# Kernel optimization log

Hardware: AMD Instinct MI355X
Metric: run time of the kernel (lower is better)

## Reference

```python
import jax, jax.numpy as jnp
import numpy as np

HEAD_SIZE = 64

def setup_inputs() -> dict:
    key = jax.random.key(0)
    kx, kk, kq, kv = jax.random.split(key, 4)
    B, T, C, H = 8, 2048, 1024, HEAD_SIZE
    scale = 1.0 / np.sqrt(C)
    x = jax.random.normal(kx, (B, T, C), dtype=jnp.float32)
    # nn.Linear(n_emb, head_size, bias=False) weights, shape (head_size, n_emb)
    Wk = jax.random.normal(kk, (H, C), dtype=jnp.float32) * scale
    Wq = jax.random.normal(kq, (H, C), dtype=jnp.float32) * scale
    Wv = jax.random.normal(kv, (H, C), dtype=jnp.float32) * scale
    return {"x": x, "Wk": Wk, "Wq": Wq, "Wv": Wv}

def reference(x, Wk, Wq, Wv):
    # x: (B,T,C); W*: (H,C). Single causal self-attention head.
    H = Wk.shape[0]
    k = jnp.einsum('btc,hc->bth', x, Wk)
    q = jnp.einsum('btc,hc->bth', x, Wq)
    v = jnp.einsum('btc,hc->bth', x, Wv)
    scores = jnp.einsum('bth,bsh->bts', q, k) / jnp.sqrt(jnp.float32(H))
    T = x.shape[1]
    causal = jnp.tril(jnp.ones((T, T), dtype=bool))  # (T,T)
    scores = jnp.where(causal, scores, -jnp.inf)
    attn = jax.nn.softmax(scores, axis=-1)
    out = jnp.einsum('bts,bsh->bth', attn, v)  # (B,T,H)
    return out
```

## Files before the change

### kernel.cpp

```cpp
#include <hip/hip_runtime.h>
#include <hip/hip_bf16.h>

typedef __bf16 bf16_t;
typedef __bf16 bf16x8 __attribute__((ext_vector_type(8)));
typedef float  f32x4  __attribute__((ext_vector_type(4)));

#define B_ 8
#define T_ 2048
#define C_ 1024
#define H_ 64

#define MFMA16(a, b, c) __builtin_amdgcn_mfma_f32_16x16x32_bf16((a), (b), (c), 0, 0, 0)
#define GLL16(g, l) __builtin_amdgcn_global_load_lds( \
    (const __attribute__((address_space(1))) unsigned int*)(g), \
    (__attribute__((address_space(3))) unsigned int*)(l), 16, 0, 0)
#define SBAR() asm volatile("s_barrier" ::: "memory")

__global__ __launch_bounds__(256) void wconv_kernel(
    const float* __restrict__ Wk, const float* __restrict__ Wq,
    const float* __restrict__ Wv,
    bf16_t* __restrict__ Wh, bf16_t* __restrict__ Wl,
    f32x4* __restrict__ zero_dst)
{
    int i = blockIdx.x * 256 + threadIdx.x;
    zero_dst[i] = (f32x4){0.f, 0.f, 0.f, 0.f};
    if (blockIdx.x < 768) {
        int r = i >> 10;
        int c = i & 1023;
        float v;
        if (r < 64)       v = Wq[r * 1024 + c];
        else if (r < 128) v = Wk[(r - 64) * 1024 + c];
        else              v = Wv[(r - 128) * 1024 + c];
        bf16_t h = (bf16_t)v;
        Wh[i] = h;
        Wl[i] = (bf16_t)(v - (float)h);
    }
}

__global__ __launch_bounds__(512, 2) void proj_kernel(
    const float*  __restrict__ x,
    const bf16_t* __restrict__ Wh, const bf16_t* __restrict__ Wl,
    bf16_t* __restrict__ qh, bf16_t* __restrict__ ql,
    bf16_t* __restrict__ kh, bf16_t* __restrict__ kl,
    bf16_t* __restrict__ vh)
{
    __shared__ bf16_t Wlds[2][48][512];

    const int tid   = threadIdx.x;
    const int wid   = tid >> 6;
    const int lane  = tid & 63;
    const int quad  = lane >> 4;
    const int l16   = lane & 15;
    const int mhalf = wid >> 1;
    const int nhalf = wid & 1;
    const int g     = blockIdx.x * 64 + mhalf * 16 + l16;
    const float* xrow = x + (size_t)g * C_;

    auto stage = [&](int k0, int bufi) {
        #pragma unroll
        for (int i = 0; i < 6; ++i) {
            int grp  = wid * 6 + i;
            int ksub = (grp >= 24);
            int rem  = grp - ksub * 24;
            int mat  = (rem >= 12);
            int nt   = rem - mat * 12;
            const bf16_t* src = (mat ? Wl : Wh)
                + (nt * 16 + l16) * 1024 + k0 + ksub * 32 + quad * 8;
            GLL16(src, &Wlds[bufi][grp][0]);
        }
    };
    auto loadx = [&](int it, f32x4* d) {
        #pragma unroll
        for (int ks = 0; ks < 2; ++ks) {
            d[ks * 2]     = *(const f32x4*)(xrow + it * 64 + ks * 32 + quad * 8);
            d[ks * 2 + 1] = *(const f32x4*)(xrow + it * 64 + ks * 32 + quad * 8 + 4);
        }
    };

    stage(0, 0);
    f32x4 x0[4], x1[4];
    loadx(0, x0);
    loadx(1, x1);

    f32x4 acc[6];
    #pragma unroll
    for (int i = 0; i < 6; ++i) acc[i] = (f32x4){0.f, 0.f, 0.f, 0.f};

    int buf = 0;
    for (int it = 0; it < 16; ++it) {
        float xv[16];
        *(f32x4*)(xv)      = x0[0];
        *(f32x4*)(xv + 4)  = x0[1];
        *(f32x4*)(xv + 8)  = x0[2];
        *(f32x4*)(xv + 12) = x0[3];
        #pragma unroll
        for (int i = 0; i < 4; ++i) x0[i] = x1[i];

        if (it + 1 < 16) {
            stage((it + 1) * 64, buf ^ 1);
            if (it + 2 < 16) {
                loadx(it + 2, x1);
                asm volatile("s_waitcnt vmcnt(10)" ::: "memory");
            } else {
                asm volatile("s_waitcnt vmcnt(6)" ::: "memory");
            }
        } else {
            asm volatile("s_waitcnt vmcnt(0)" ::: "memory");
        }
        SBAR();

        #pragma unroll
        for (int ks = 0; ks < 2; ++ks) {
            bf16x8 ah, al;
            #pragma unroll
            for (int jj = 0; jj < 8; ++jj) {
                float  xf = xv[ks * 8 + jj];
                bf16_t h  = (bf16_t)xf;
                ah[jj] = h;
                al[jj] = (bf16_t)(xf - (float)h);
            }
            #pragma unroll
            for (int nt = 0; nt < 6; ++nt) {
                int gi = ks * 24 + nhalf * 6 + nt;
                bf16x8 bh = *(const bf16x8*)(&Wlds[buf][gi][lane * 8]);
                bf16x8 bl = *(const bf16x8*)(&Wlds[buf][gi + 12][lane * 8]);
                acc[nt] = MFMA16(ah, bh, acc[nt]);
                acc[nt] = MFMA16(ah, bl, acc[nt]);
                acc[nt] = MFMA16(al, bh, acc[nt]);
            }
        }

        SBAR();
        buf ^= 1;
    }

    const int rowbase = blockIdx.x * 64 + mhalf * 16 + quad * 4;
    for (int nt = 0; nt < 6; ++nt) {
        int n = (nhalf * 6 + nt) * 16 + l16;
        for (int rr = 0; rr < 4; ++rr) {
            int grow = rowbase + rr;
            int bb = grow >> 11, t = grow & 2047;
            float v  = acc[nt][rr];
            bf16_t h = (bf16_t)v;
            if (n < 64) {
                int off = (bb * T_ + t) * H_ + n;
                qh[off] = h; ql[off] = (bf16_t)(v - (float)h);
            } else if (n < 128) {
                int off = (bb * T_ + t) * H_ + (n - 64);
                kh[off] = h; kl[off] = (bf16_t)(v - (float)h);
            } else {
                vh[(bb * H_ + (n - 128)) * T_ + t] = h;
            }
        }
    }
}

__global__ __launch_bounds__(512, 4) void attn_kernel(
    const bf16_t* __restrict__ qh, const bf16_t* __restrict__ ql,
    const bf16_t* __restrict__ kh, const bf16_t* __restrict__ kl,
    const bf16_t* __restrict__ vh,
    float* __restrict__ Oacc, float* __restrict__ lacc)
{
    __shared__ bf16_t KV[2][3][4096];
    __shared__ bf16_t Plds[8][16 * 72];

    const int tid  = threadIdx.x;
    const int wid  = tid >> 6;
    const int lane = tid & 63;
    const int quad = lane >> 4;
    const int l16  = lane & 15;

    const int b  = blockIdx.x & 7;
    const int gp = (blockIdx.x >> 3) & 7;
    const int s  = blockIdx.x >> 6;
    const int gA = gp, gB = 15 - gp;
    const int nA = 2 * gA + 2;

    const int t_nt   = wid >> 1;
    const int t_kk   = wid & 1;
    const int t_l16  = tid & 15;
    const int t_quad = (tid >> 4) & 3;
    const int koff   = (t_nt * 16 + t_l16) * H_ + t_kk * 32 + t_quad * 8;
    const int voff   = (t_nt * 16 + t_l16) * T_ + t_kk * 32 + t_quad * 8;

    auto stage = [&](int j, int bufi) {
        const size_t kbase = (size_t)(b * T_ + 64 * j) * H_;
        GLL16(kh + kbase + koff, &KV[bufi][0][wid * 512]);
        GLL16(kl + kbase + koff, &KV[bufi][1][wid * 512]);
        GLL16(vh + (size_t)b * H_ * T_ + 64 * j + voff, &KV[bufi][2][wid * 512]);
    };

    f32x4  O[4];
    float  rowsum[4];
    bf16x8 aqh[2], aql[2];
    int    gcur = -1;

    auto flushO = [&]() {
        #pragma unroll
        for (int rr = 0; rr < 4; ++rr) {
            int trow = b * T_ + 128 * gcur + 16 * wid + quad * 4 + rr;
            #pragma unroll
            for (int ht = 0; ht < 4; ++ht)
                atomicAdd(Oacc + (size_t)trow * H_ + ht * 16 + l16, O[ht][rr]);
            float s_ = rowsum[rr];
            s_ += __shfl_xor(s_, 1, 64);
            s_ += __shfl_xor(s_, 2, 64);
            s_ += __shfl_xor(s_, 4, 64);
            s_ += __shfl_xor(s_, 8, 64);
            if (l16 == 0) atomicAdd(lacc + trow, s_);
        }
    };

    {
        int u0 = s;
        int j0 = (u0 < nA) ? u0 : (u0 - nA);
        stage(j0, 0);
    }

    int buf = 0;
    for (int u = s; u < 34; u += 8) {
        const int g = (u < nA) ? gA : gB;
        const int j = (u < nA) ? u : (u - nA);

        const int un = u + 8;
        if (un < 34) {
            int jn = (un < nA) ? un : (un - nA);
            stage(jn, buf ^ 1);
            asm volatile("s_waitcnt vmcnt(3)" ::: "memory");
        } else {
            asm volatile("s_waitcnt vmcnt(0)" ::: "memory");
        }
        SBAR();

        if (g != gcur) {
            if (gcur >= 0) flushO();
            gcur = g;
            const size_t qoff = (size_t)(b * T_ + 128 * g + 16 * wid + l16) * H_;
            #pragma unroll
            for (int kk = 0; kk < 2; ++kk) {
                aqh[kk] = *(const bf16x8*)(qh + qoff + kk * 32 + quad * 8);
                aql[kk] = *(const bf16x8*)(ql + qoff + kk * 32 + quad * 8);
            }
            #pragma unroll
            for (int i = 0; i < 4; ++i) { O[i] = (f32x4){0.f,0.f,0.f,0.f}; rowsum[i] = 0.f; }
        }

        const bf16_t* Kh = KV[buf][0];
        const bf16_t* Kl = KV[buf][1];
        f32x4 S[4];
        #pragma unroll
        for (int i = 0; i < 4; ++i) S[i] = (f32x4){0.f,0.f,0.f,0.f};
        #pragma unroll
        for (int nt = 0; nt < 4; ++nt) {
            #pragma unroll
            for (int kk = 0; kk < 2; ++kk) {
                bf16x8 bh = *(const bf16x8*)(Kh + (nt * 2 + kk) * 512 + lane * 8);
                bf16x8 bl = *(const bf16x8*)(Kl + (nt * 2 + kk) * 512 + lane * 8);
                S[nt] = MFMA16(aqh[kk], bh, S[nt]);
                S[nt] = MFMA16(aqh[kk], bl, S[nt]);
                S[nt] = MFMA16(aql[kk], bh, S[nt]);
            }
        }

        bf16_t* Pw = Plds[wid];
        const int rloc = 128 * g + 16 * wid + quad * 4;
        #pragma unroll
        for (int nt = 0; nt < 4; ++nt) {
            int colt = 64 * j + nt * 16 + l16;
            #pragma unroll
            for (int rr = 0; rr < 4; ++rr) {
                float pv = (colt <= rloc + rr)
                         ? __expf(fmaf(S[nt][rr], 0.125f, -20.0f)) : 0.f;
                rowsum[rr] += pv;
                Pw[(quad * 4 + rr) * 72 + nt * 16 + l16] = (bf16_t)pv;
            }
        }

        bf16x8 ap0 = *(const bf16x8*)(Pw + l16 * 72 + quad * 8);
        bf16x8 ap1 = *(const bf16x8*)(Pw + l16 * 72 + 32 + quad * 8);

        const bf16_t* Vt = KV[buf][2];
        #pragma unroll
        for (int ht = 0; ht < 4; ++ht) {
            bf16x8 bv0 = *(const bf16x8*)(Vt + (ht * 2 + 0) * 512 + lane * 8);
            bf16x8 bv1 = *(const bf16x8*)(Vt + (ht * 2 + 1) * 512 + lane * 8);
            O[ht] = MFMA16(ap0, bv0, O[ht]);
            O[ht] = MFMA16(ap1, bv1, O[ht]);
        }

        SBAR();
        buf ^= 1;
    }
    if (gcur >= 0) flushO();
}

__global__ __launch_bounds__(256) void div_kernel(
    const float* __restrict__ Oacc, const float* __restrict__ lacc,
    float* __restrict__ out)
{
    int i = blockIdx.x * 256 + threadIdx.x;
    f32x4 o   = ((const f32x4*)Oacc)[i];
    float inv = 1.0f / lacc[i >> 4];
    ((f32x4*)out)[i] = o * inv;
}

extern "C" void kernel_launch(void* const* d_in, const int* in_sizes, int n_in,
                              void* d_out, int out_size, void* d_ws, size_t ws_size,
                              hipStream_t stream)
{
    const float* x  = (const float*)d_in[0];
    const float* Wk = (const float*)d_in[1];
    const float* Wq = (const float*)d_in[2];
    const float* Wv = (const float*)d_in[3];
    float* out = (float*)d_out;

    char* ws = (char*)d_ws;
    const size_t WSZ = 192 * 1024 * sizeof(bf16_t);
    const size_t QSZ = (size_t)B_ * T_ * H_ * sizeof(bf16_t);
    bf16_t* Wh   = (bf16_t*)(ws);
    bf16_t* Wl   = (bf16_t*)(ws + WSZ);
    bf16_t* qh   = (bf16_t*)(ws + 2 * WSZ);
    bf16_t* ql   = (bf16_t*)(ws + 2 * WSZ + 1 * QSZ);
    bf16_t* kh   = (bf16_t*)(ws + 2 * WSZ + 2 * QSZ);
    bf16_t* kl   = (bf16_t*)(ws + 2 * WSZ + 3 * QSZ);
    bf16_t* vh   = (bf16_t*)(ws + 2 * WSZ + 4 * QSZ);
    float*  Oacc = (float*)(ws + 2 * WSZ + 5 * QSZ);
    float*  lacc = (float*)(ws + 2 * WSZ + 5 * QSZ + (size_t)B_ * T_ * H_ * 4);

    hipLaunchKernelGGL(wconv_kernel, dim3(1040), dim3(256), 0, stream,
                       Wk, Wq, Wv, Wh, Wl, (f32x4*)Oacc);
    hipLaunchKernelGGL(proj_kernel, dim3(256), dim3(512), 0, stream,
                       x, Wh, Wl, qh, ql, kh, kl, vh);
    hipLaunchKernelGGL(attn_kernel, dim3(512), dim3(512), 0, stream,
                       qh, ql, kh, kl, vh, Oacc, lacc);
    hipLaunchKernelGGL(div_kernel, dim3(1024), dim3(256), 0, stream, Oacc, lacc, out);
}
```

Before: 169.9 us.

## Fuse weight bf16 split conversion and accumulator zeroing into projection kernel

Removes the separate weight-conversion kernel. The projection kernel now loads fp32 weights directly, splits them into hi/lo bf16 in registers and writes them to a triple-buffered LDS ring. Each loop iteration then needs one barrier instead of two. Zeroing of the attention accumulator moves to the end of the projection kernel. This saves a launch and a global round trip for the converted weights, but adds conversion ALU work in every block and uses full vmcnt(0) waits, which may expose more load latency.

After: 163.8 us. 3.6% less time.

```diff
diff --git a/kernel.cpp b/kernel.cpp
--- a/kernel.cpp
+++ b/kernel.cpp
@@ -16,35 +16,16 @@
     (__attribute__((address_space(3))) unsigned int*)(l), 16, 0, 0)
 #define SBAR() asm volatile("s_barrier" ::: "memory")
 
-__global__ __launch_bounds__(256) void wconv_kernel(
+__global__ __launch_bounds__(512, 2) void proj_kernel(
+    const float* __restrict__ x,
     const float* __restrict__ Wk, const float* __restrict__ Wq,
     const float* __restrict__ Wv,
-    bf16_t* __restrict__ Wh, bf16_t* __restrict__ Wl,
+    bf16_t* __restrict__ qh, bf16_t* __restrict__ ql,
+    bf16_t* __restrict__ kh, bf16_t* __restrict__ kl,
+    bf16_t* __restrict__ vh,
     f32x4* __restrict__ zero_dst)
 {
-    int i = blockIdx.x * 256 + threadIdx.x;
-    zero_dst[i] = (f32x4){0.f, 0.f, 0.f, 0.f};
-    if (blockIdx.x < 768) {
-        int r = i >> 10;
-        int c = i & 1023;
-        float v;
-        if (r < 64)       v = Wq[r * 1024 + c];
-        else if (r < 128) v = Wk[(r - 64) * 1024 + c];
-        else              v = Wv[(r - 128) * 1024 + c];
-        bf16_t h = (bf16_t)v;
-        Wh[i] = h;
-        Wl[i] = (bf16_t)(v - (float)h);
-    }
-}
-
-__global__ __launch_bounds__(512, 2) void proj_kernel(
-    const float*  __restrict__ x,
-    const bf16_t* __restrict__ Wh, const bf16_t* __restrict__ Wl,
-    bf16_t* __restrict__ qh, bf16_t* __restrict__ ql,
-    bf16_t* __restrict__ kh, bf16_t* __restrict__ kl,
-    bf16_t* __restrict__ vh)
-{
-    __shared__ bf16_t Wlds[2][48][512];
+    __shared__ bf16_t Wlds[3][48][512];
 
     const int tid   = threadIdx.x;
     const int wid   = tid >> 6;
@@ -56,17 +37,49 @@
     const int g     = blockIdx.x * 64 + mhalf * 16 + l16;
     const float* xrow = x + (size_t)g * C_;
 
-    auto stage = [&](int k0, int bufi) {
-        #pragma unroll
-        for (int i = 0; i < 6; ++i) {
-            int grp  = wid * 6 + i;
-            int ksub = (grp >= 24);
-            int rem  = grp - ksub * 24;
-            int mat  = (rem >= 12);
-            int nt   = rem - mat * 12;
-            const bf16_t* src = (mat ? Wl : Wh)
-                + (nt * 16 + l16) * 1024 + k0 + ksub * 32 + quad * 8;
-            GLL16(src, &Wlds[bufi][grp][0]);
+    const float* ck_src[3];
+    int          ck_hi[3], ck_lo[3];
+    #pragma unroll
+    for (int i = 0; i < 3; ++i) {
+        int ci   = tid + 512 * i;
+        int ksub = ci / 768;
+        int r    = ci - ksub * 768;
+        int nt   = r >> 6;
+        int ln   = r & 63;
+        int row  = nt * 16 + (ln & 15);
+        const float* base;
+        if (row < 64)       base = Wq + row * 1024;
+        else if (row < 128) base = Wk + (row - 64) * 1024;
+        else                base = Wv + (row - 128) * 1024;
+        ck_src[i] = base + ksub * 32 + (ln >> 4) * 8;
+        ck_hi[i]  = (ksub * 24 + nt) * 512 + ln * 8;
+        ck_lo[i]  = (ksub * 24 + 12 + nt) * 512 + ln * 8;
+    }
+
+    f32x4 wr[6];
+    auto loadW = [&](int it) {
+        #pragma unroll
+        for (int i = 0; i < 3; ++i) {
+            wr[i * 2]     = *(const f32x4*)(ck_src[i] + it * 64);
+            wr[i * 2 + 1] = *(const f32x4*)(ck_src[i] + it * 64 + 4);
+        }
+    };
+    auto convertWrite = [&](int slot) {
+        bf16_t* L = &Wlds[slot][0][0];
+        #pragma unroll
+        for (int i = 0; i < 3; ++i) {
+            float wf[8];
+            *(f32x4*)(wf)     = wr[i * 2];
+            *(f32x4*)(wf + 4) = wr[i * 2 + 1];
+            bf16x8 hv, lv;
+            #pragma unroll
+            for (int j = 0; j < 8; ++j) {
+                bf16_t h = (bf16_t)wf[j];
+                hv[j] = h;
+                lv[j] = (bf16_t)(wf[j] - (float)h);
+            }
+            *(bf16x8*)(L + ck_hi[i]) = hv;
+            *(bf16x8*)(L + ck_lo[i]) = lv;
         }
     };
     auto loadx = [&](int it, f32x4* d) {
@@ -77,17 +90,23 @@
         }
     };
 
-    stage(0, 0);
     f32x4 x0[4], x1[4];
+    loadW(0);
     loadx(0, x0);
     loadx(1, x1);
+    asm volatile("s_waitcnt vmcnt(0)" ::: "memory");
+    convertWrite(0);
+    loadW(1);
+    asm volatile("s_waitcnt lgkmcnt(0)" ::: "memory");
+    SBAR();
 
     f32x4 acc[6];
     #pragma unroll
     for (int i = 0; i < 6; ++i) acc[i] = (f32x4){0.f, 0.f, 0.f, 0.f};
 
-    int buf = 0;
     for (int it = 0; it < 16; ++it) {
+        const int slot = it % 3;
+
         float xv[16];
         *(f32x4*)(xv)      = x0[0];
         *(f32x4*)(xv + 4)  = x0[1];
@@ -96,17 +115,16 @@
         #pragma unroll
         for (int i = 0; i < 4; ++i) x0[i] = x1[i];
 
+        asm volatile("s_waitcnt vmcnt(0)" ::: "memory");
+
         if (it + 1 < 16) {
-            stage((it + 1) * 64, buf ^ 1);
+            convertWrite((it + 1) % 3);
             if (it + 2 < 16) {
+                loadW(it + 2);
                 loadx(it + 2, x1);
-                asm volatile("s_waitcnt vmcnt(10)" ::: "memory");
-            } else {
-                asm volatile("s_waitcnt vmcnt(6)" ::: "memory");
-            }
-        } else {
-            asm volatile("s_waitcnt vmcnt(0)" ::: "memory");
-        }
+            }
+        }
+        asm volatile("s_waitcnt lgkmcnt(0)" ::: "memory");
         SBAR();
 
         #pragma unroll
@@ -122,16 +140,13 @@
             #pragma unroll
             for (int nt = 0; nt < 6; ++nt) {
                 int gi = ks * 24 + nhalf * 6 + nt;
-                bf16x8 bh = *(const bf16x8*)(&Wlds[buf][gi][lane * 8]);
-                bf16x8 bl = *(const bf16x8*)(&Wlds[buf][gi + 12][lane * 8]);
+                bf16x8 bh = *(const bf16x8*)(&Wlds[slot][gi][lane * 8]);
+                bf16x8 bl = *(const bf16x8*)(&Wlds[slot][gi + 12][lane * 8]);
                 acc[nt] = MFMA16(ah, bh, acc[nt]);
                 acc[nt] = MFMA16(ah, bl, acc[nt]);
                 acc[nt] = MFMA16(al, bh, acc[nt]);
             }
         }
-
-        SBAR();
-        buf ^= 1;
     }
 
     const int rowbase = blockIdx.x * 64 + mhalf * 16 + quad * 4;
@@ -153,6 +168,12 @@
             }
         }
     }
+
+    {
+        f32x4* Z = zero_dst + (size_t)blockIdx.x * 1040;
+        for (int i = tid; i < 1040; i += 512)
+            Z[i] = (f32x4){0.f, 0.f, 0.f, 0.f};
+    }
 }
 
 __global__ __launch_bounds__(512, 4) void attn_kernel(
@@ -315,22 +336,17 @@
     float* out = (float*)d_out;
 
     char* ws = (char*)d_ws;
-    const size_t WSZ = 192 * 1024 * sizeof(bf16_t);
     const size_t QSZ = (size_t)B_ * T_ * H_ * sizeof(bf16_t);
-    bf16_t* Wh   = (bf16_t*)(ws);
-    bf16_t* Wl   = (bf16_t*)(ws + WSZ);
-    bf16_t* qh   = (bf16_t*)(ws + 2 * WSZ);
-    bf16_t* ql   = (bf16_t*)(ws + 2 * WSZ + 1 * QSZ);
-    bf16_t* kh   = (bf16_t*)(ws + 2 * WSZ + 2 * QSZ);
-    bf16_t* kl   = (bf16_t*)(ws + 2 * WSZ + 3 * QSZ);
-    bf16_t* vh   = (bf16_t*)(ws + 2 * WSZ + 4 * QSZ);
-    float*  Oacc = (float*)(ws + 2 * WSZ + 5 * QSZ);
-    float*  lacc = (float*)(ws + 2 * WSZ + 5 * QSZ + (size_t)B_ * T_ * H_ * 4);
-
-    hipLaunchKernelGGL(wconv_kernel, dim3(1040), dim3(256), 0, stream,
-                       Wk, Wq, Wv, Wh, Wl, (f32x4*)Oacc);
+    bf16_t* qh   = (bf16_t*)(ws);
+    bf16_t* ql   = (bf16_t*)(ws + 1 * QSZ);
+    bf16_t* kh   = (bf16_t*)(ws + 2 * QSZ);
+    bf16_t* kl   = (bf16_t*)(ws + 3 * QSZ);
+    bf16_t* vh   = (bf16_t*)(ws + 4 * QSZ);
+    float*  Oacc = (float*)(ws + 5 * QSZ);
+    float*  lacc = (float*)(ws + 5 * QSZ + (size_t)B_ * T_ * H_ * 4);
+
     hipLaunchKernelGGL(proj_kernel, dim3(256), dim3(512), 0, stream,
-                       x, Wh, Wl, qh, ql, kh, kl, vh);
+                       x, Wk, Wq, Wv, qh, ql, kh, kl, vh, (f32x4*)Oacc);
     hipLaunchKernelGGL(attn_kernel, dim3(512), dim3(512), 0, stream,
                        qh, ql, kh, kl, vh, Oacc, lacc);
     hipLaunchKernelGGL(div_kernel, dim3(1024), dim3(256), 0, stream, Oacc, lacc, out);
```
